# Optimization experiments

Measured on AMD Instinct MI355X. Metric: run time of the kernel, lower is better.

## Reference

```python
import jax, jax.numpy as jnp
import numpy as np

GLM_HIDDEN = 256
POS_EMB_DIM = 64
LN_EPS = 1e-5


def _pair_indices(seq_len, K):
    # emo index i (row), cau index j (col); keep |j-i| <= K (static mask)
    i = np.repeat(np.arange(seq_len), seq_len)
    j = np.tile(np.arange(seq_len), seq_len)
    rel = j - i
    keep = np.abs(rel) <= K
    return i[keep], j[keep], rel[keep]


def setup_inputs() -> dict:
    key = jax.random.key(0)
    ks = jax.random.split(key, 8)
    B, S, D, P, K = 32, 128, GLM_HIDDEN, POS_EMB_DIM, 8
    doc_sents_h = jax.random.normal(ks[0], (B, S, D), dtype=jnp.float32)
    pos_emb = jax.random.normal(ks[1], (2 * K + 1, P), dtype=jnp.float32) * 0.1
    in_dim = 2 * D + P
    W1 = jax.random.normal(ks[2], (D, in_dim), dtype=jnp.float32) * (1.0 / np.sqrt(in_dim))
    b1 = jnp.zeros((D,), dtype=jnp.float32)
    ln_g = jnp.ones((D,), dtype=jnp.float32)
    ln_b = jnp.zeros((D,), dtype=jnp.float32)
    W2 = jax.random.normal(ks[3], (1, D), dtype=jnp.float32) * (1.0 / np.sqrt(D))
    b2 = jnp.zeros((1,), dtype=jnp.float32)
    return {"doc_sents_h": doc_sents_h, "pos_emb": pos_emb, "W1": W1, "b1": b1,
            "ln_g": ln_g, "ln_b": ln_b, "W2": W2, "b2": b2, "K": K}


def reference(doc_sents_h, pos_emb, W1, b1, ln_g, ln_b, W2, b2, K):
    B, S, D = doc_sents_h.shape
    ii, jj, rel = _pair_indices(S, K)          # static numpy, shape [n_couple]
    # couples = [H_i ; H_j] for in-window pairs (replaces broadcast-concat + masked_select)
    couples = jnp.concatenate([doc_sents_h[:, ii], doc_sents_h[:, jj]], axis=-1)  # [B,n,2D]
    rel_idx = jnp.asarray(rel + K, dtype=jnp.int32)
    rpe = pos_emb[rel_idx]                     # [n, P]
    rf = jnp.asarray(rel, dtype=jnp.float32)
    kernel = jnp.exp(-jnp.square(rf[:, None] - rf[None, :]))  # [n, n]
    rpe = kernel @ rpe                         # [n, P] (same for every batch elem)
    pair = jnp.concatenate(
        [couples, jnp.broadcast_to(rpe[None], (B,) + rpe.shape)], axis=-1)  # [B,n,2D+P]
    h = jnp.einsum('bnf,df->bnd', pair, W1) + b1
    mu = jnp.mean(h, axis=-1, keepdims=True)
    var = jnp.mean(jnp.square(h - mu), axis=-1, keepdims=True)
    h = (h - mu) * jax.lax.rsqrt(var + LN_EPS) * ln_g + ln_b
    h = jax.nn.elu(h)                          # dropout is identity in eval
    scores = (jnp.einsum('bnd,od->bno', h, W2) + b2)[..., 0]  # [B, n]
    emo_cau_pos = jnp.stack([jnp.asarray(ii + 1), jnp.asarray(jj + 1)], axis=1)  # [n, 2]
    return scores, emo_cau_pos
```

## Files before the change

### kernel.cpp

```cpp
#include <hip/hip_runtime.h>
#include <math.h>

constexpr int kB = 32;
constexpr int kS = 128;
constexpr int kD = 256;
constexpr int kK = 8;
constexpr int kNPair = 2104;
constexpr int kInDim = 576;
constexpr int kRS = 264;

typedef __attribute__((ext_vector_type(8))) short short8;
typedef __attribute__((ext_vector_type(4))) float f32x4;

__device__ inline ushort f2b(float f) {
  union { float f; uint u; } v; v.f = f;
  uint r = v.u + 0x7FFF + ((v.u >> 16) & 1);
  return (ushort)(r >> 16);
}

__global__ __launch_bounds__(256, 1) void fused_all(
    const float* __restrict__ H, const float* __restrict__ pos_emb,
    const float* __restrict__ W1, const float* __restrict__ b1,
    const float* __restrict__ ln_g, const float* __restrict__ ln_b,
    const float* __restrict__ W2, const float* __restrict__ b2,
    float* __restrict__ out) {
  __shared__ __align__(16) ushort sH[48 * 256];
  __shared__ __align__(16) ushort sW[64 * 256];
  __shared__ __align__(16) ushort sKpe[32 * 64];
  __shared__ float sU[16 * kRS];
  __shared__ float sV[48 * kRS];
  __shared__ float sR[17 * kRS];
  __shared__ float sG[256], sBe[256], sWo[256], sB1[256];
  __shared__ float sB2v;

  const int tid = threadIdx.x;
  const int b = blockIdx.x >> 3;
  const int i0 = (blockIdx.x & 7) << 4;
  int ws_ = i0 - 16; if (ws_ < 0) ws_ = 0; if (ws_ > 80) ws_ = 80;
  const int ws = ws_;
  const int oi = i0 - ws;

  sG[tid] = ln_g[tid]; sBe[tid] = ln_b[tid]; sWo[tid] = W2[tid]; sB1[tid] = b1[tid];
  if (tid == 0) sB2v = b2[0];

#pragma unroll
  for (int l = 0; l < 12; ++l) {
    int c = tid + l * 256, row = c >> 6, kq = (c & 63) << 2;
    float4 a4 = *(const float4*)(H + (b * kS + ws + row) * kD + kq);
    ushort4 u; u.x = f2b(a4.x); u.y = f2b(a4.y); u.z = f2b(a4.z); u.w = f2b(a4.w);
    *(ushort4*)&sH[row * 256 + (kq ^ ((row & 7) << 3))] = u;
  }
#pragma unroll
  for (int l = 0; l < 16; ++l) {
    int c = tid + l * 256, d = c >> 4, kq = (c & 15) << 2;
    float4 a4 = *(const float4*)(W1 + d * kInDim + 512 + kq);
    ushort4 u; u.x = f2b(a4.x); u.y = f2b(a4.y); u.z = f2b(a4.z); u.w = f2b(a4.w);
    *(ushort4*)&sW[d * 64 + (kq ^ ((d & 7) << 3))] = u;
  }
  {
    const int pg = (tid & 15) << 2;
#pragma unroll
    for (int pass = 0; pass < 2; ++pass) {
      int t = (tid >> 4) + pass * 16;
      float a0 = 0.f, a1 = 0.f, a2 = 0.f, a3 = 0.f;
      if (t < 17) {
        for (int u = 0; u < 17; ++u) {
          int du = t - u, au = u - kK; if (au < 0) au = -au;
          float wt = __expf((float)(-(du * du))) * (float)(kS - au);
          float4 pe = *(const float4*)(pos_emb + u * 64 + pg);
          a0 += wt * pe.x; a1 += wt * pe.y; a2 += wt * pe.z; a3 += wt * pe.w;
        }
      }
      ushort4 u; u.x = f2b(a0); u.y = f2b(a1); u.z = f2b(a2); u.w = f2b(a3);
      *(ushort4*)&sKpe[t * 64 + (pg ^ ((t & 7) << 3))] = u;
    }
  }
  __syncthreads();

  const int lane = tid & 63;
  const int w = tid >> 6;
  const int lr = lane & 15;
  const int lk = (lane >> 4) << 3;
  const int swz = (lr & 7) << 3;
  const int r0 = (lane >> 4) << 2;

  {
    f32x4 racc[2][4] = {{{0,0,0,0},{0,0,0,0},{0,0,0,0},{0,0,0,0}},
                        {{0,0,0,0},{0,0,0,0},{0,0,0,0},{0,0,0,0}}};
#pragma unroll
    for (int kk = 0; kk < 2; ++kk) {
      int k0 = (kk << 5) + lk;
      short8 a0 = *(const short8*)(const void*)&sKpe[lr * 64 + (k0 ^ swz)];
      short8 a1 = *(const short8*)(const void*)&sKpe[(16 + lr) * 64 + (k0 ^ swz)];
#pragma unroll
      for (int n = 0; n < 4; ++n) {
        int drow = ((w << 2) + n) * 16 + lr;
        short8 bf = *(const short8*)(const void*)&sW[drow * 64 + (k0 ^ swz)];
        racc[0][n] = __builtin_amdgcn_mfma_f32_16x16x32_bf16(a0, bf, racc[0][n], 0, 0, 0);
        racc[1][n] = __builtin_amdgcn_mfma_f32_16x16x32_bf16(a1, bf, racc[1][n], 0, 0, 0);
      }
    }
#pragma unroll
    for (int m = 0; m < 2; ++m)
#pragma unroll
      for (int r = 0; r < 4; ++r) {
        int t = m * 16 + r0 + r;
        if (t < 17) {
#pragma unroll
          for (int n = 0; n < 4; ++n) {
            int d = ((w << 2) + n) * 16 + lr;
            sR[t * kRS + d] = racc[m][n][r] + sB1[d];
          }
        }
      }
  }
  __syncthreads();

  for (int nt = 0; nt < 8; ++nt) {
#pragma unroll
    for (int l = 0; l < 16; ++l) {
      int c = tid + l * 256, row = c >> 6, kq = (c & 63) << 2;
      int cg = (nt << 6) + row;
      const float* src = W1 + (cg & 255) * kInDim + ((cg < 256) ? 0 : 256) + kq;
      float4 a4 = *(const float4*)src;
      ushort4 u; u.x = f2b(a4.x); u.y = f2b(a4.y); u.z = f2b(a4.z); u.w = f2b(a4.w);
      *(ushort4*)&sW[row * 256 + (kq ^ ((row & 7) << 3))] = u;
    }
    __syncthreads();
    f32x4 acc[3] = {{0,0,0,0},{0,0,0,0},{0,0,0,0}};
    const int brow = (w << 4) + lr;
#pragma unroll
    for (int kk = 0; kk < 8; ++kk) {
      int k0 = (kk << 5) + lk;
      short8 bf = *(const short8*)(const void*)&sW[brow * 256 + (k0 ^ swz)];
#pragma unroll
      for (int m = 0; m < 3; ++m) {
        short8 af = *(const short8*)(const void*)&sH[(m * 16 + lr) * 256 + (k0 ^ swz)];
        acc[m] = __builtin_amdgcn_mfma_f32_16x16x32_bf16(af, bf, acc[m], 0, 0, 0);
      }
    }
    const int cg = (nt << 6) + (w << 4) + lr;
#pragma unroll
    for (int m = 0; m < 3; ++m)
#pragma unroll
      for (int r = 0; r < 4; ++r) {
        int rw = m * 16 + r0 + r;
        float val = acc[m][r];
        if (cg < 256) {
          unsigned ur = (unsigned)(rw - oi);
          if (ur < 16u) sU[ur * kRS + cg] = val;
        } else {
          sV[rw * kRS + (cg - 256)] = val;
        }
      }
    __syncthreads();
  }

  const int g = tid >> 4, l16 = tid & 15;
  float4 Gp[4], Bp[4], Wp[4];
#pragma unroll
  for (int q = 0; q < 4; ++q) {
    int d = (q << 6) + (l16 << 2);
    Gp[q] = *(const float4*)&sG[d];
    Bp[q] = *(const float4*)&sBe[d];
    Wp[q] = *(const float4*)&sWo[d];
  }
  const float bias2 = sB2v;

  for (int s = g; s < 272; s += 16) {
    int ir = s / 17, t = s - ir * 17;
    int i = i0 + ir, j = i - kK + t;
    if (j < 0 || j >= kS) continue;
    int vr = j - ws;
    int start_i;
    if (i <= 8)        start_i = (i * i + 17 * i) / 2;
    else if (i <= 120) start_i = 100 + (i - 8) * 17;
    else { int m = i - 120; start_i = 2004 + 16 * m - (m * (m - 1)) / 2; }
    const int lower = (i - kK > 0) ? (i - kK) : 0;
    const int p = start_i + (j - lower);

    const float* Ur = &sU[ir * kRS];
    const float* Vr = &sV[vr * kRS];
    const float* Rr = &sR[t * kRS];
    float h[16]; float ssum = 0.f, qsum = 0.f;
#pragma unroll
    for (int q = 0; q < 4; ++q) {
      int d = (q << 6) + (l16 << 2);
      float4 u4 = *(const float4*)(Ur + d);
      float4 v4 = *(const float4*)(Vr + d);
      float4 r4 = *(const float4*)(Rr + d);
      float h0 = u4.x + v4.x + r4.x;
      float h1 = u4.y + v4.y + r4.y;
      float h2 = u4.z + v4.z + r4.z;
      float h3 = u4.w + v4.w + r4.w;
      h[q * 4 + 0] = h0; h[q * 4 + 1] = h1; h[q * 4 + 2] = h2; h[q * 4 + 3] = h3;
      ssum += h0 + h1 + h2 + h3;
      qsum += h0 * h0 + h1 * h1 + h2 * h2 + h3 * h3;
    }
#pragma unroll
    for (int off = 8; off > 0; off >>= 1) {
      ssum += __shfl_xor(ssum, off);
      qsum += __shfl_xor(qsum, off);
    }
    const float mu = ssum * (1.0f / kD);
    const float var = qsum * (1.0f / kD) - mu * mu;
    const float rs = rsqrtf(var + 1e-5f);
    float dot = 0.f;
#pragma unroll
    for (int q = 0; q < 4; ++q) {
      float y0 = (h[q * 4 + 0] - mu) * rs * Gp[q].x + Bp[q].x;
      float y1 = (h[q * 4 + 1] - mu) * rs * Gp[q].y + Bp[q].y;
      float y2 = (h[q * 4 + 2] - mu) * rs * Gp[q].z + Bp[q].z;
      float y3 = (h[q * 4 + 3] - mu) * rs * Gp[q].w + Bp[q].w;
      y0 = y0 > 0.f ? y0 : (__expf(y0) - 1.0f);
      y1 = y1 > 0.f ? y1 : (__expf(y1) - 1.0f);
      y2 = y2 > 0.f ? y2 : (__expf(y2) - 1.0f);
      y3 = y3 > 0.f ? y3 : (__expf(y3) - 1.0f);
      dot += y0 * Wp[q].x + y1 * Wp[q].y + y2 * Wp[q].z + y3 * Wp[q].w;
    }
#pragma unroll
    for (int off = 8; off > 0; off >>= 1) dot += __shfl_xor(dot, off);

    if (l16 == 0) {
      out[b * kNPair + p] = dot + bias2;
      if (b == 0) {
        float* po = out + kB * kNPair;
        po[2 * p + 0] = (float)(i + 1);
        po[2 * p + 1] = (float)(j + 1);
      }
    }
  }
}

extern "C" void kernel_launch(void* const* d_in, const int* in_sizes, int n_in,
                              void* d_out, int out_size, void* d_ws, size_t ws_size,
                              hipStream_t stream) {
  (void)in_sizes; (void)n_in; (void)d_ws; (void)ws_size; (void)out_size;
  const float* H       = (const float*)d_in[0];
  const float* pos_emb = (const float*)d_in[1];
  const float* W1      = (const float*)d_in[2];
  const float* b1      = (const float*)d_in[3];
  const float* ln_g    = (const float*)d_in[4];
  const float* ln_b    = (const float*)d_in[5];
  const float* W2      = (const float*)d_in[6];
  const float* b2      = (const float*)d_in[7];
  float* out = (float*)d_out;

  fused_all<<<kB * 8, 256, 0, stream>>>(H, pos_emb, W1, b1, ln_g, ln_b, W2, b2, out);
}
```

Before: 39.95 us.

## Split bf16 preconversion into prep kernel and stream weights via async LDS loads

A separate prep kernel converts H and the W1 halves to swizzled bf16 in workspace once, and computes the relative-position bias table (kernel @ pos_emb @ W1 slice + b1) in fp32 instead of bf16 MFMA. The main kernel then uses global_load_lds to copy the pre-swizzled tiles directly into shared memory, prefetching the next W tile while the current results are written. It also runs with 512 threads, only 4 of which waves do MFMA, and restructures the epilogue so each thread group keeps its U row in registers. This removes redundant per-block fp32-to-bf16 conversion and R computation, at the cost of an extra launch and workspace round trip.

Result: slower. 46.15 us (+15.5%).

```diff
diff --git a/kernel.cpp b/kernel.cpp
--- a/kernel.cpp
+++ b/kernel.cpp
@@ -11,6 +11,7 @@
 
 typedef __attribute__((ext_vector_type(8))) short short8;
 typedef __attribute__((ext_vector_type(4))) float f32x4;
+typedef unsigned int u32;
 
 __device__ inline ushort f2b(float f) {
   union { float f; uint u; } v; v.f = f;
@@ -18,145 +19,163 @@
   return (ushort)(r >> 16);
 }
 
-__global__ __launch_bounds__(256, 1) void fused_all(
+__device__ inline void gload16(const void* g, void* lds) {
+  __builtin_amdgcn_global_load_lds(
+      (const u32 __attribute__((address_space(1)))*)g,
+      (u32 __attribute__((address_space(3)))*)lds, 16, 0, 0);
+}
+
+__global__ __launch_bounds__(256) void prep(
     const float* __restrict__ H, const float* __restrict__ pos_emb,
     const float* __restrict__ W1, const float* __restrict__ b1,
+    ushort* __restrict__ Hb, ushort* __restrict__ Wb, float* __restrict__ Rg) {
+  const int blk = blockIdx.x, tid = threadIdx.x;
+  if (blk < 256) {
+#pragma unroll
+    for (int l = 0; l < 4; ++l) {
+      int c = blk * 1024 + l * 256 + tid;
+      int row = c >> 6, kq = (c & 63) << 2;
+      float4 a = *(const float4*)(H + row * kD + kq);
+      ushort4 u; u.x = f2b(a.x); u.y = f2b(a.y); u.z = f2b(a.z); u.w = f2b(a.w);
+      *(ushort4*)(Hb + row * 256 + (kq ^ ((row & 7) << 3))) = u;
+    }
+  } else if (blk < 288) {
+    int bb = blk - 256;
+#pragma unroll
+    for (int l = 0; l < 4; ++l) {
+      int c = bb * 1024 + l * 256 + tid;
+      int r = c >> 6;
+      int kq = (c & 63) << 2;
+      int nt = r >> 6, rr = r & 63;
+      const float* src = W1 + (r & 255) * kInDim + ((r < 256) ? 0 : 256) + kq;
+      float4 a = *(const float4*)src;
+      ushort4 u; u.x = f2b(a.x); u.y = f2b(a.y); u.z = f2b(a.z); u.w = f2b(a.w);
+      *(ushort4*)(Wb + (nt * 64 + rr) * 256 + (kq ^ ((rr & 7) << 3))) = u;
+    }
+  } else {
+    __shared__ float pe[17 * 64];
+    for (int idx = tid; idx < 17 * 64; idx += 256) pe[idx] = pos_emb[idx];
+    __syncthreads();
+    const int d = tid;
+    float w[64];
+    const float* wr = W1 + d * kInDim + 512;
+#pragma unroll
+    for (int q = 0; q < 16; ++q) {
+      float4 t4 = *(const float4*)(wr + q * 4);
+      w[q * 4 + 0] = t4.x; w[q * 4 + 1] = t4.y;
+      w[q * 4 + 2] = t4.z; w[q * 4 + 3] = t4.w;
+    }
+    float acc[17];
+#pragma unroll
+    for (int t = 0; t < 17; ++t) acc[t] = 0.f;
+    for (int u = 0; u < 17; ++u) {
+      float m = 0.f;
+#pragma unroll
+      for (int p = 0; p < 64; ++p) m += pe[u * 64 + p] * w[p];
+      int au = u - kK; if (au < 0) au = -au;
+      m *= (float)(kS - au);
+#pragma unroll
+      for (int t = 0; t < 17; ++t) {
+        int dd = t - u;
+        acc[t] += expf((float)(-(dd * dd))) * m;
+      }
+    }
+#pragma unroll
+    for (int t = 0; t < 17; ++t) Rg[t * kD + d] = acc[t] + b1[d];
+  }
+}
+
+__global__ __launch_bounds__(512, 2) void fused2(
+    const ushort* __restrict__ Hb, const ushort* __restrict__ Wb,
+    const float* __restrict__ Rg,
     const float* __restrict__ ln_g, const float* __restrict__ ln_b,
     const float* __restrict__ W2, const float* __restrict__ b2,
     float* __restrict__ out) {
   __shared__ __align__(16) ushort sH[48 * 256];
   __shared__ __align__(16) ushort sW[64 * 256];
-  __shared__ __align__(16) ushort sKpe[32 * 64];
   __shared__ float sU[16 * kRS];
   __shared__ float sV[48 * kRS];
   __shared__ float sR[17 * kRS];
-  __shared__ float sG[256], sBe[256], sWo[256], sB1[256];
-  __shared__ float sB2v;
+  __shared__ float sG[256], sBe[256], sWo[256];
 
   const int tid = threadIdx.x;
+  const int lane = tid & 63;
   const int b = blockIdx.x >> 3;
   const int i0 = (blockIdx.x & 7) << 4;
   int ws_ = i0 - 16; if (ws_ < 0) ws_ = 0; if (ws_ > 80) ws_ = 80;
   const int ws = ws_;
   const int oi = i0 - ws;
 
-  sG[tid] = ln_g[tid]; sBe[tid] = ln_b[tid]; sWo[tid] = W2[tid]; sB1[tid] = b1[tid];
-  if (tid == 0) sB2v = b2[0];
-
-#pragma unroll
-  for (int l = 0; l < 12; ++l) {
-    int c = tid + l * 256, row = c >> 6, kq = (c & 63) << 2;
-    float4 a4 = *(const float4*)(H + (b * kS + ws + row) * kD + kq);
-    ushort4 u; u.x = f2b(a4.x); u.y = f2b(a4.y); u.z = f2b(a4.z); u.w = f2b(a4.w);
-    *(ushort4*)&sH[row * 256 + (kq ^ ((row & 7) << 3))] = u;
-  }
-#pragma unroll
-  for (int l = 0; l < 16; ++l) {
-    int c = tid + l * 256, d = c >> 4, kq = (c & 15) << 2;
-    float4 a4 = *(const float4*)(W1 + d * kInDim + 512 + kq);
-    ushort4 u; u.x = f2b(a4.x); u.y = f2b(a4.y); u.z = f2b(a4.z); u.w = f2b(a4.w);
-    *(ushort4*)&sW[d * 64 + (kq ^ ((d & 7) << 3))] = u;
-  }
   {
-    const int pg = (tid & 15) << 2;
-#pragma unroll
-    for (int pass = 0; pass < 2; ++pass) {
-      int t = (tid >> 4) + pass * 16;
-      float a0 = 0.f, a1 = 0.f, a2 = 0.f, a3 = 0.f;
-      if (t < 17) {
-        for (int u = 0; u < 17; ++u) {
-          int du = t - u, au = u - kK; if (au < 0) au = -au;
-          float wt = __expf((float)(-(du * du))) * (float)(kS - au);
-          float4 pe = *(const float4*)(pos_emb + u * 64 + pg);
-          a0 += wt * pe.x; a1 += wt * pe.y; a2 += wt * pe.z; a3 += wt * pe.w;
-        }
-      }
-      ushort4 u; u.x = f2b(a0); u.y = f2b(a1); u.z = f2b(a2); u.w = f2b(a3);
-      *(ushort4*)&sKpe[t * 64 + (pg ^ ((t & 7) << 3))] = u;
-    }
+    const ushort* src = Hb + (b * kS + ws) * 256;
+    for (int idx = tid; idx < 1536; idx += 512)
+      gload16(src + idx * 8, (char*)sH + (idx - lane) * 16);
+  }
+  for (int idx = tid; idx < 2048; idx += 512)
+    gload16(Wb + idx * 8, (char*)sW + (idx - lane) * 16);
+  if (tid < 256) { sG[tid] = ln_g[tid]; sBe[tid] = ln_b[tid]; sWo[tid] = W2[tid]; }
+  for (int idx = tid; idx < 1088; idx += 512) {
+    float4 a = *(const float4*)(Rg + idx * 4);
+    int t = idx >> 6, d = (idx & 63) << 2;
+    *(float4*)&sR[t * kRS + d] = a;
   }
   __syncthreads();
 
-  const int lane = tid & 63;
   const int w = tid >> 6;
   const int lr = lane & 15;
   const int lk = (lane >> 4) << 3;
   const int swz = (lr & 7) << 3;
   const int r0 = (lane >> 4) << 2;
 
-  {
-    f32x4 racc[2][4] = {{{0,0,0,0},{0,0,0,0},{0,0,0,0},{0,0,0,0}},
-                        {{0,0,0,0},{0,0,0,0},{0,0,0,0},{0,0,0,0}}};
-#pragma unroll
-    for (int kk = 0; kk < 2; ++kk) {
-      int k0 = (kk << 5) + lk;
-      short8 a0 = *(const short8*)(const void*)&sKpe[lr * 64 + (k0 ^ swz)];
-      short8 a1 = *(const short8*)(const void*)&sKpe[(16 + lr) * 64 + (k0 ^ swz)];
-#pragma unroll
-      for (int n = 0; n < 4; ++n) {
-        int drow = ((w << 2) + n) * 16 + lr;
-        short8 bf = *(const short8*)(const void*)&sW[drow * 64 + (k0 ^ swz)];
-        racc[0][n] = __builtin_amdgcn_mfma_f32_16x16x32_bf16(a0, bf, racc[0][n], 0, 0, 0);
-        racc[1][n] = __builtin_amdgcn_mfma_f32_16x16x32_bf16(a1, bf, racc[1][n], 0, 0, 0);
-      }
-    }
-#pragma unroll
-    for (int m = 0; m < 2; ++m)
-#pragma unroll
-      for (int r = 0; r < 4; ++r) {
-        int t = m * 16 + r0 + r;
-        if (t < 17) {
-#pragma unroll
-          for (int n = 0; n < 4; ++n) {
-            int d = ((w << 2) + n) * 16 + lr;
-            sR[t * kRS + d] = racc[m][n][r] + sB1[d];
-          }
+  for (int nt = 0; nt < 8; ++nt) {
+    f32x4 acc[3] = {{0,0,0,0},{0,0,0,0},{0,0,0,0}};
+    if (w < 4) {
+      const int brow = (w << 4) + lr;
+#pragma unroll
+      for (int kk = 0; kk < 8; ++kk) {
+        int k0 = (kk << 5) + lk;
+        short8 bf = *(const short8*)(const void*)&sW[brow * 256 + (k0 ^ swz)];
+#pragma unroll
+        for (int m = 0; m < 3; ++m) {
+          short8 af = *(const short8*)(const void*)&sH[(m * 16 + lr) * 256 + (k0 ^ swz)];
+          acc[m] = __builtin_amdgcn_mfma_f32_16x16x32_bf16(af, bf, acc[m], 0, 0, 0);
         }
       }
-  }
-  __syncthreads();
-
-  for (int nt = 0; nt < 8; ++nt) {
-#pragma unroll
-    for (int l = 0; l < 16; ++l) {
-      int c = tid + l * 256, row = c >> 6, kq = (c & 63) << 2;
-      int cg = (nt << 6) + row;
-      const float* src = W1 + (cg & 255) * kInDim + ((cg < 256) ? 0 : 256) + kq;
-      float4 a4 = *(const float4*)src;
-      ushort4 u; u.x = f2b(a4.x); u.y = f2b(a4.y); u.z = f2b(a4.z); u.w = f2b(a4.w);
-      *(ushort4*)&sW[row * 256 + (kq ^ ((row & 7) << 3))] = u;
     }
     __syncthreads();
-    f32x4 acc[3] = {{0,0,0,0},{0,0,0,0},{0,0,0,0}};
-    const int brow = (w << 4) + lr;
-#pragma unroll
-    for (int kk = 0; kk < 8; ++kk) {
-      int k0 = (kk << 5) + lk;
-      short8 bf = *(const short8*)(const void*)&sW[brow * 256 + (k0 ^ swz)];
-#pragma unroll
-      for (int m = 0; m < 3; ++m) {
-        short8 af = *(const short8*)(const void*)&sH[(m * 16 + lr) * 256 + (k0 ^ swz)];
-        acc[m] = __builtin_amdgcn_mfma_f32_16x16x32_bf16(af, bf, acc[m], 0, 0, 0);
-      }
-    }
-    const int cg = (nt << 6) + (w << 4) + lr;
-#pragma unroll
-    for (int m = 0; m < 3; ++m)
-#pragma unroll
-      for (int r = 0; r < 4; ++r) {
-        int rw = m * 16 + r0 + r;
-        float val = acc[m][r];
-        if (cg < 256) {
-          unsigned ur = (unsigned)(rw - oi);
-          if (ur < 16u) sU[ur * kRS + cg] = val;
-        } else {
-          sV[rw * kRS + (cg - 256)] = val;
+    if (nt < 7) {
+      const ushort* src = Wb + (nt + 1) * 16384;
+      for (int idx = tid; idx < 2048; idx += 512)
+        gload16(src + idx * 8, (char*)sW + (idx - lane) * 16);
+    }
+    if (w < 4) {
+      const int cg = (nt << 6) + (w << 4) + lr;
+#pragma unroll
+      for (int m = 0; m < 3; ++m)
+#pragma unroll
+        for (int r = 0; r < 4; ++r) {
+          int rw = m * 16 + r0 + r;
+          float val = acc[m][r];
+          if (cg < 256) { unsigned ur = (unsigned)(rw - oi); if (ur < 16u) sU[ur * kRS + cg] = val; }
+          else sV[rw * kRS + (cg - 256)] = val;
         }
-      }
+    }
     __syncthreads();
   }
 
   const int g = tid >> 4, l16 = tid & 15;
+  const int ir = g >> 1;
+  const int tbeg = (g & 1) ? 9 : 0;
+  const int tend = (g & 1) ? 17 : 9;
+  const int i = i0 + ir;
+
+  float ureg[16];
+#pragma unroll
+  for (int q = 0; q < 4; ++q) {
+    float4 u4 = *(const float4*)&sU[ir * kRS + (q << 6) + (l16 << 2)];
+    ureg[q * 4 + 0] = u4.x; ureg[q * 4 + 1] = u4.y;
+    ureg[q * 4 + 2] = u4.z; ureg[q * 4 + 3] = u4.w;
+  }
   float4 Gp[4], Bp[4], Wp[4];
 #pragma unroll
   for (int q = 0; q < 4; ++q) {
@@ -165,34 +184,32 @@
     Bp[q] = *(const float4*)&sBe[d];
     Wp[q] = *(const float4*)&sWo[d];
   }
-  const float bias2 = sB2v;
-
-  for (int s = g; s < 272; s += 16) {
-    int ir = s / 17, t = s - ir * 17;
-    int i = i0 + ir, j = i - kK + t;
+  const float bias2 = b2[0];
+
+  int start_i;
+  if (i <= 8)        start_i = (i * i + 17 * i) / 2;
+  else if (i <= 120) start_i = 100 + (i - 8) * 17;
+  else { int m = i - 120; start_i = 2004 + 16 * m - (m * (m - 1)) / 2; }
+  const int lower = (i - kK > 0) ? (i - kK) : 0;
+
+  for (int t = tbeg; t < tend; ++t) {
+    int j = i - kK + t;
     if (j < 0 || j >= kS) continue;
-    int vr = j - ws;
-    int start_i;
-    if (i <= 8)        start_i = (i * i + 17 * i) / 2;
-    else if (i <= 120) start_i = 100 + (i - 8) * 17;
-    else { int m = i - 120; start_i = 2004 + 16 * m - (m * (m - 1)) / 2; }
-    const int lower = (i - kK > 0) ? (i - kK) : 0;
+    const int vr = j - ws;
     const int p = start_i + (j - lower);
-
-    const float* Ur = &sU[ir * kRS];
     const float* Vr = &sV[vr * kRS];
     const float* Rr = &sR[t * kRS];
+
     float h[16]; float ssum = 0.f, qsum = 0.f;
 #pragma unroll
     for (int q = 0; q < 4; ++q) {
       int d = (q << 6) + (l16 << 2);
-      float4 u4 = *(const float4*)(Ur + d);
       float4 v4 = *(const float4*)(Vr + d);
       float4 r4 = *(const float4*)(Rr + d);
-      float h0 = u4.x + v4.x + r4.x;
-      float h1 = u4.y + v4.y + r4.y;
-      float h2 = u4.z + v4.z + r4.z;
-      float h3 = u4.w + v4.w + r4.w;
+      float h0 = ureg[q * 4 + 0] + v4.x + r4.x;
+      float h1 = ureg[q * 4 + 1] + v4.y + r4.y;
+      float h2 = ureg[q * 4 + 2] + v4.z + r4.z;
+      float h3 = ureg[q * 4 + 3] + v4.w + r4.w;
       h[q * 4 + 0] = h0; h[q * 4 + 1] = h1; h[q * 4 + 2] = h2; h[q * 4 + 3] = h3;
       ssum += h0 + h1 + h2 + h3;
       qsum += h0 * h0 + h1 * h1 + h2 * h2 + h3 * h3;
@@ -235,7 +252,7 @@
 extern "C" void kernel_launch(void* const* d_in, const int* in_sizes, int n_in,
                               void* d_out, int out_size, void* d_ws, size_t ws_size,
                               hipStream_t stream) {
-  (void)in_sizes; (void)n_in; (void)d_ws; (void)ws_size; (void)out_size;
+  (void)in_sizes; (void)n_in; (void)ws_size; (void)out_size;
   const float* H       = (const float*)d_in[0];
   const float* pos_emb = (const float*)d_in[1];
   const float* W1      = (const float*)d_in[2];
@@ -246,5 +263,10 @@
   const float* b2      = (const float*)d_in[7];
   float* out = (float*)d_out;
 
-  fused_all<<<kB * 8, 256, 0, stream>>>(H, pos_emb, W1, b1, ln_g, ln_b, W2, b2, out);
-}
+  ushort* Hb = (ushort*)d_ws;
+  ushort* Wb = Hb + 4096 * 256;
+  float*  Rg = (float*)(Wb + 512 * 256);
+
+  prep<<<289, 256, 0, stream>>>(H, pos_emb, W1, b1, Hb, Wb, Rg);
+  fused2<<<kB * 8, 512, 0, stream>>>(Hb, Wb, Rg, ln_g, ln_b, W2, b2, out);
+}
```
